# Kernel tuning notes

Hardware: AMD Instinct MI355X
Metric: run time of the kernel (lower is better)

The kernel has to match this reference:

```python
import jax, jax.numpy as jnp
import numpy as np

N_NODES = 50000
N_EDGES = 800000
IN_F = 128
HID = 128
N_REL = 8


def setup_inputs() -> dict:
    key = jax.random.key(0)
    ks = jax.random.split(key, 12)
    s = 0.05
    return {
        "in_feat": jax.random.normal(ks[0], (N_NODES, IN_F), dtype=jnp.float32),
        "W1": jax.random.normal(ks[1], (N_REL, IN_F, HID), dtype=jnp.float32) * s,
        "W1_self": jax.random.normal(ks[2], (IN_F, HID), dtype=jnp.float32) * s,
        "b1": jnp.zeros((HID,), dtype=jnp.float32),
        "W2": jax.random.normal(ks[3], (N_REL, HID, HID), dtype=jnp.float32) * s,
        "W2_self": jax.random.normal(ks[4], (HID, HID), dtype=jnp.float32) * s,
        "b2": jnp.zeros((HID,), dtype=jnp.float32),
        "fc_w": jax.random.normal(ks[5], (HID, 1), dtype=jnp.float32) * s,
        "fc_b": jnp.zeros((1,), dtype=jnp.float32),
        "src": jax.random.randint(ks[6], (N_EDGES,), 0, N_NODES),
        "dst": jax.random.randint(ks[7], (N_EDGES,), 0, N_NODES),
        "etypes": jax.random.randint(ks[8], (N_EDGES,), 0, N_REL),
    }


def _rel_graph_conv(h, W, W_self, b, src, dst, etypes, n_nodes):
    # Transform node features once per relation: [R, N, H]
    xr = jnp.einsum('nd,rdh->rnh', h, W)
    # Per-edge message: gather relation-specific transformed source features [E, H]
    msgs = xr[etypes, src]
    # Scatter-sum aggregation to destination nodes [N, H]
    agg = jax.ops.segment_sum(msgs, dst, num_segments=n_nodes)
    # Self-loop + bias + ReLU (DGL RelGraphConv defaults)
    return jax.nn.relu(agg + h @ W_self + b)


def reference(in_feat, W1, W1_self, b1, W2, W2_self, b2, fc_w, fc_b, src, dst, etypes):
    n = in_feat.shape[0]
    h = _rel_graph_conv(in_feat, W1, W1_self, b1, src, dst, etypes, n)
    # dropout layers are identity in eval mode
    h = _rel_graph_conv(h, W2, W2_self, b2, src, dst, etypes, n)
    pooled = jnp.mean(h, axis=0, keepdims=True)  # AvgPooling over one graph -> [1, H]
    logits = pooled @ fc_w + fc_b                # [1, 1]
    return jax.nn.sigmoid(logits)
```

## Files before the change

### kernel.cpp

```cpp
#include <hip/hip_runtime.h>

#define NNODES 50000
#define NEDGES 800000
#define F 128
#define NREL 8
#define NOUT 1152
#define NBKT 98
#define BSH 9
#define SEG 16384
#define NTILES 391
#define GEMM_BLOCKS (8 * 9 * 49)
#define CSR_BLOCKS 196

typedef float f32x4 __attribute__((ext_vector_type(4)));
typedef float f32x2 __attribute__((ext_vector_type(2)));

typedef __attribute__((address_space(3))) void lds_void;
typedef const __attribute__((address_space(1))) void glb_void;
__device__ __forceinline__ void gll16(const void* g, void* l) {
  __builtin_amdgcn_global_load_lds(
      (glb_void*)(unsigned long long)g,
      (lds_void*)(unsigned)(unsigned long long)l, 16, 0, 0);
}

#define PREP_ZERO  33
#define PREP_CVT   6250
#define PREP_W     144
__global__ __launch_bounds__(256)
void k_prep(const float* __restrict__ in_feat, unsigned* __restrict__ feat0,
            const float* __restrict__ W1, const float* __restrict__ W1s,
            unsigned* __restrict__ Wt1,
            const float* __restrict__ W2, const float* __restrict__ W2s,
            unsigned* __restrict__ Wt2,
            float* __restrict__ pooled_p, int* __restrict__ bcur) {
  const int b = blockIdx.x, t = threadIdx.x;
  if (b < 32) {
    pooled_p[b * 256 + t] = 0.f;
  } else if (b < PREP_ZERO) {
    if (t <= NBKT) bcur[t] = 0;
  } else if (b < PREP_ZERO + PREP_CVT) {
    int i = (b - PREP_ZERO) * 256 + t;
    float4 v = ((const float4*)in_feat)[i];
    unsigned pk = 0;
    pk = __builtin_amdgcn_cvt_pk_fp8_f32(v.x, v.y, pk, false);
    pk = __builtin_amdgcn_cvt_pk_fp8_f32(v.z, v.w, pk, true);
    feat0[i] = pk;
  } else {
    int w2 = (b >= PREP_ZERO + PREP_CVT + PREP_W);
    int idx = (b - PREP_ZERO - PREP_CVT - (w2 ? PREP_W : 0)) * 256 + t;
    int n = idx >> 5, k0 = (idx & 31) * 4;
    int r = n >> 7, c = n & 127;
    const float* Wr = w2 ? W2 : W1;
    const float* Ws = w2 ? W2s : W1s;
    float v0, v1, v2, v3;
    if (r < NREL) {
      v0 = Wr[((size_t)(r * F + k0 + 0)) * F + c];
      v1 = Wr[((size_t)(r * F + k0 + 1)) * F + c];
      v2 = Wr[((size_t)(r * F + k0 + 2)) * F + c];
      v3 = Wr[((size_t)(r * F + k0 + 3)) * F + c];
    } else {
      v0 = Ws[(size_t)(k0 + 0) * F + c];
      v1 = Ws[(size_t)(k0 + 1) * F + c];
      v2 = Ws[(size_t)(k0 + 2) * F + c];
      v3 = Ws[(size_t)(k0 + 3) * F + c];
    }
    unsigned pk = 0;
    pk = __builtin_amdgcn_cvt_pk_fp8_f32(v0, v1, pk, false);
    pk = __builtin_amdgcn_cvt_pk_fp8_f32(v2, v3, pk, true);
    (w2 ? Wt2 : Wt1)[idx] = pk;
  }
}

__global__ __launch_bounds__(512)
void k_fsort(const int* __restrict__ ebuf, const int* __restrict__ bcur,
             int* __restrict__ rowptr, int* __restrict__ edata) {
  __shared__ int cnt[512];
  __shared__ int pos[512];
  __shared__ int ws2[512];
  __shared__ int bc_s;
  const int b = blockIdx.x, t = threadIdx.x;
  int myc = (t < NBKT) ? bcur[t] : 0;
  ws2[t] = (t < b) ? myc : 0;
  if (t == b) bc_s = myc;
  __syncthreads();
  for (int off = 1; off < 512; off <<= 1) {
    int x = (t >= off) ? ws2[t - off] : 0;
    __syncthreads();
    ws2[t] += x;
    __syncthreads();
  }
  const int beg = ws2[511];
  const int cntb = bc_s;
  const int sbeg = b * SEG;

  cnt[t] = 0;
  __syncthreads();
  for (int e = t; e < cntb; e += 512)
    atomicAdd(&cnt[((unsigned)ebuf[sbeg + e]) >> 19], 1);
  __syncthreads();
  int myn = cnt[t];
  ws2[t] = myn;
  __syncthreads();
  for (int off = 1; off < 512; off <<= 1) {
    int x = (t >= off) ? ws2[t - off] : 0;
    __syncthreads();
    ws2[t] += x;
    __syncthreads();
  }
  pos[t] = ws2[t] - myn;
  __syncthreads();
  int node = (b << BSH) + t;
  if (node < NNODES) rowptr[node] = beg + pos[t];
  if (b == NBKT - 1 && t == 0) rowptr[NNODES] = NEDGES;
  __syncthreads();
  for (int e = t; e < cntb; e += 512) {
    int rec = ebuf[sbeg + e];
    int c = ((unsigned)rec) >> 19;
    int lrank = atomicAdd(&pos[c], 1);
    int srcv = (rec >> 3) & 0xFFFF;
    int etv = rec & 7;
    edata[beg + lrank] = srcv * NOUT + etv * F;
  }
}

__global__ __launch_bounds__(512, 8)
void gemm_xrs(const unsigned char* __restrict__ A,
              const unsigned char* __restrict__ Wt,
              unsigned char* __restrict__ xrs, int doCsr,
              const int* __restrict__ src, const int* __restrict__ dst,
              const int* __restrict__ et, int* __restrict__ bcur,
              int* __restrict__ ebuf) {
  __shared__ uint4 As[1024];
  __shared__ uint4 Bs[1024];
  __shared__ int lhist[NBKT];
  __shared__ int lbase[NBKT];
  const int tid = threadIdx.x;

  if (doCsr && blockIdx.x < CSR_BLOCKS) {
    if (tid < NBKT) lhist[tid] = 0;
    __syncthreads();
    int e0 = blockIdx.x * 4096;
    int rec[8], cc[8], lr[8];
#pragma unroll
    for (int i = 0; i < 8; ++i) {
      int e = e0 + tid + i * 512;
      if (e < NEDGES) {
        int d = dst[e];
        cc[i] = d >> BSH;
        rec[i] = ((d & 511) << 19) | (src[e] << 3) | et[e];
        lr[i] = atomicAdd(&lhist[cc[i]], 1);
      } else {
        cc[i] = -1;
      }
    }
    __syncthreads();
    if (tid < NBKT && lhist[tid] > 0) lbase[tid] = atomicAdd(&bcur[tid], lhist[tid]);
    __syncthreads();
#pragma unroll
    for (int i = 0; i < 8; ++i)
      if (cc[i] >= 0) ebuf[cc[i] * SEG + lbase[cc[i]] + lr[i]] = rec[i];
    return;
  }

  const int id = blockIdx.x - (doCsr ? CSR_BLOCKS : 0);
  const int x = id & 7, j = id >> 3;
  const int tile = (j / 9) * 8 + x;
  const int cb = j % 9;
  if (tile >= NTILES) return;
  const int row0 = tile * 128;

  const int lane = tid & 63;
  const int w = tid >> 6;
  const int i16 = lane & 15, q = lane >> 4;
  const int mbase = (w & 3) * 32, nbase = (w >> 2) * 64;

#pragma unroll
  for (int i = 0; i < 2; ++i) {
    int L = tid + i * 512;
    int r = L >> 3, c8s = L & 7;
    int c8 = c8s ^ (r & 7);
    int agr = row0 + r; if (agr >= NNODES) agr = NNODES - 1;
    gll16((const void*)(A + (size_t)agr * F + c8 * 16), (void*)&As[L]);
    gll16((const void*)(Wt + ((size_t)cb * 128 + r) * F + c8 * 16), (void*)&Bs[L]);
  }
  __syncthreads();

  f32x4 acc[2][4];
#pragma unroll
  for (int a = 0; a < 2; ++a)
#pragma unroll
    for (int b = 0; b < 4; ++b) acc[a][b] = (f32x4)0.f;

  const char* Ab = (const char*)As;
  const char* Bb = (const char*)Bs;
#pragma unroll
  for (int c = 0; c < 4; ++c) {
    const int ch = c * 2 + (q >> 1);
    const int h8 = (q & 1) << 3;
    long af[2], bfr[4];
#pragma unroll
    for (int mi = 0; mi < 2; ++mi) {
      int r = mbase + mi * 16 + i16;
      af[mi] = *(const long*)(Ab + r * 128 + ((ch ^ (r & 7)) << 4) + h8);
    }
#pragma unroll
    for (int ni = 0; ni < 4; ++ni) {
      int r = nbase + ni * 16 + i16;
      bfr[ni] = *(const long*)(Bb + r * 128 + ((ch ^ (r & 7)) << 4) + h8);
    }
#pragma unroll
    for (int mi = 0; mi < 2; ++mi)
#pragma unroll
      for (int ni = 0; ni < 4; ++ni)
        acc[mi][ni] = __builtin_amdgcn_mfma_f32_16x16x32_fp8_fp8(
            bfr[ni], af[mi], acc[mi][ni], 0, 0, 0);
  }

  unsigned pkv[2][4];
#pragma unroll
  for (int mi = 0; mi < 2; ++mi)
#pragma unroll
    for (int ni = 0; ni < 4; ++ni) {
      f32x4 v = acc[mi][ni];
      unsigned pk = 0;
      pk = __builtin_amdgcn_cvt_pk_fp8_f32(v[0], v[1], pk, false);
      pk = __builtin_amdgcn_cvt_pk_fp8_f32(v[2], v[3], pk, true);
      pkv[mi][ni] = pk;
    }

  __syncthreads();
  unsigned* sbuf = (unsigned*)As;
  {
    const int dbase = (nbase >> 2) + q;
#pragma unroll
    for (int mi = 0; mi < 2; ++mi) {
      int nl = mbase + mi * 16 + i16;
      int sw = (nl & 7) << 2;
      int vb_ = nl * 32;
#pragma unroll
      for (int ni = 0; ni < 4; ++ni)
        sbuf[vb_ + ((dbase + ni * 4) ^ sw)] = pkv[mi][ni];
    }
  }
  __syncthreads();

#pragma unroll
  for (int k = 0; k < 2; ++k) {
    int nl = k * 64 + (tid >> 3);
    int ch = tid & 7;
    int d0 = (ch * 4) ^ ((nl & 7) << 2);
    uint4 v = *(const uint4*)&sbuf[nl * 32 + d0];
    int row = row0 + nl;
    if (row < NNODES)
      *(uint4*)(xrs + (size_t)row * NOUT + cb * 128 + ch * 16) = v;
  }
}

__global__ __launch_bounds__(256)
void k_aggregate(const unsigned char* __restrict__ xrs,
                 const int* __restrict__ rowptr, const int* __restrict__ edata,
                 const float* __restrict__ bias, unsigned char* __restrict__ hout,
                 float* __restrict__ pooled_p) {
  __shared__ float red[8][128];
  const int wv = threadIdx.x >> 6;
  const int lane = threadIdx.x & 63;
  const int h = lane >> 5;
  const int sl = lane & 31;
  const int g = sl >> 3, s8 = sl & 7;
  const int node = blockIdx.x * 8 + wv * 2 + h;
  const int beg = rowptr[node], end = rowptr[node + 1];

  float a[16];
#pragma unroll
  for (int j = 0; j < 16; ++j) a[j] = 0.f;

#define ACC4(word, o_) { \
    f32x2 lo_ = __builtin_amdgcn_cvt_pk_f32_fp8((word), false); \
    f32x2 hi_ = __builtin_amdgcn_cvt_pk_f32_fp8((word), true);  \
    a[(o_) + 0] += lo_[0]; a[(o_) + 1] += lo_[1];               \
    a[(o_) + 2] += hi_[0]; a[(o_) + 3] += hi_[1]; }
#define ACC16(v_) { ACC4((v_).x, 0) ACC4((v_).y, 4) ACC4((v_).z, 8) ACC4((v_).w, 12) }

  if (g == 0) {
    uint4 sv = *(const uint4*)(xrs + (size_t)node * NOUT + NREL * F + s8 * 16);
    ACC16(sv)
  }

  for (int base = beg; base < end; base += 32) {
    int cnt = end - base; if (cnt > 32) cnt = 32;
    int my = (base + sl < end) ? edata[base + sl] : 0;
    int nfull = cnt >> 2, tail = cnt & 3;
    for (int qb = 0; qb < nfull; qb += 8) {
      int nq = nfull - qb; if (nq > 8) nq = 8;
      uint4 v[8];
#pragma unroll
      for (int k = 0; k < 8; ++k) {
        if (k < nq) {
          int off = __shfl(my, 4 * (qb + k) + g, 32);
          v[k] = *(const uint4*)(xrs + (size_t)off + s8 * 16);
        }
      }
#pragma unroll
      for (int k = 0; k < 8; ++k) {
        if (k < nq) ACC16(v[k])
      }
    }
    if (tail) {
      int e = 4 * nfull + g;
      int off = __shfl(my, (e < cnt) ? e : 0, 32);
      if (g < tail) {
        uint4 vv = *(const uint4*)(xrs + (size_t)off + s8 * 16);
        ACC16(vv)
      }
    }
  }

#pragma unroll
  for (int j = 0; j < 16; ++j) {
    a[j] += __shfl_xor(a[j], 8, 64);
    a[j] += __shfl_xor(a[j], 16, 64);
  }

#pragma unroll
  for (int i = 0; i < 4; ++i) {
    float4 bb = ((const float4*)bias)[s8 * 4 + i];
    a[i * 4 + 0] = fmaxf(a[i * 4 + 0] + bb.x, 0.f);
    a[i * 4 + 1] = fmaxf(a[i * 4 + 1] + bb.y, 0.f);
    a[i * 4 + 2] = fmaxf(a[i * 4 + 2] + bb.z, 0.f);
    a[i * 4 + 3] = fmaxf(a[i * 4 + 3] + bb.w, 0.f);
  }

  if (hout) {
    if (g == 0) {
      unsigned pk[4];
#pragma unroll
      for (int i = 0; i < 4; ++i) {
        unsigned p = 0;
        p = __builtin_amdgcn_cvt_pk_fp8_f32(a[i * 4 + 0], a[i * 4 + 1], p, false);
        p = __builtin_amdgcn_cvt_pk_fp8_f32(a[i * 4 + 2], a[i * 4 + 3], p, true);
        pk[i] = p;
      }
      *(uint4*)(hout + (size_t)node * F + s8 * 16) =
          make_uint4(pk[0], pk[1], pk[2], pk[3]);
    }
  } else {
    if (g == 0) {
#pragma unroll
      for (int j = 0; j < 16; ++j) red[wv * 2 + h][s8 * 16 + j] = a[j];
    }
    __syncthreads();
    if (threadIdx.x < 128) {
      float sm = 0.f;
#pragma unroll
      for (int r = 0; r < 8; ++r) sm += red[r][threadIdx.x];
      atomicAdd(&pooled_p[(blockIdx.x & 63) * 128 + threadIdx.x], sm);
    }
  }
#undef ACC16
#undef ACC4
}

__global__ __launch_bounds__(128)
void k_final(const float* __restrict__ pooled_p, const float* __restrict__ fcw,
             const float* __restrict__ fcb, float* __restrict__ out) {
  __shared__ float s[128];
  int t = threadIdx.x;
  float acc = 0.f;
#pragma unroll 8
  for (int k = 0; k < 64; ++k) acc += pooled_p[k * 128 + t];
  s[t] = acc * (1.0f / (float)NNODES) * fcw[t];
  __syncthreads();
  if (t == 0) {
    float v = 0.f;
    for (int i = 0; i < 128; ++i) v += s[i];
    v += fcb[0];
    out[0] = 1.f / (1.f + expf(-v));
  }
}

extern "C" void kernel_launch(void* const* d_in, const int* in_sizes, int n_in,
                              void* d_out, int out_size, void* d_ws, size_t ws_size,
                              hipStream_t stream) {
  const float* in_feat = (const float*)d_in[0];
  const float* W1      = (const float*)d_in[1];
  const float* W1s     = (const float*)d_in[2];
  const float* b1      = (const float*)d_in[3];
  const float* W2      = (const float*)d_in[4];
  const float* W2s     = (const float*)d_in[5];
  const float* b2      = (const float*)d_in[6];
  const float* fcw     = (const float*)d_in[7];
  const float* fcb     = (const float*)d_in[8];
  const int*   src     = (const int*)d_in[9];
  const int*   dst     = (const int*)d_in[10];
  const int*   et      = (const int*)d_in[11];
  float* out = (float*)d_out;

  unsigned char* xrs = (unsigned char*)d_ws;
  unsigned char* feat0 = xrs + (size_t)NNODES * NOUT;
  unsigned char* h1  = feat0 + (size_t)NNODES * F;
  unsigned char* Wt1 = h1 + (size_t)NNODES * F;
  unsigned char* Wt2 = Wt1 + (size_t)NOUT * F;
  float* pooled_p = (float*)(Wt2 + (size_t)NOUT * F);
  int*   bcur   = (int*)(pooled_p + 64 * 128);
  int*   rowptr = bcur + NBKT + 1;
  int*   ebuf   = rowptr + NNODES + 2;
  int*   edata  = ebuf + NBKT * SEG;

  k_prep<<<PREP_ZERO + PREP_CVT + 2 * PREP_W, 256, 0, stream>>>(
      in_feat, (unsigned*)feat0, W1, W1s, (unsigned*)Wt1,
      W2, W2s, (unsigned*)Wt2, pooled_p, bcur);

  const int aggBlocks = NNODES / 8;

  gemm_xrs<<<CSR_BLOCKS + GEMM_BLOCKS, 512, 0, stream>>>(
      feat0, Wt1, xrs, 1, src, dst, et, bcur, ebuf);
  k_fsort<<<NBKT, 512, 0, stream>>>(ebuf, bcur, rowptr, edata);
  k_aggregate<<<aggBlocks, 256, 0, stream>>>(xrs, rowptr, edata, b1, h1, nullptr);
  gemm_xrs<<<GEMM_BLOCKS, 512, 0, stream>>>(
      h1, Wt2, xrs, 0, src, dst, et, bcur, ebuf);
  k_aggregate<<<aggBlocks, 256, 0, stream>>>(xrs, rowptr, edata, b2, nullptr, pooled_p);

  k_final<<<1, 128, 0, stream>>>(pooled_p, fcw, fcb, out);
}
```

Baseline: 198.9 us.

## Move edge bucketing into prep and fuse CSR sort into first GEMM launch

Edge bucketing by destination moves from the first GEMM launch into the prep kernel. The per-bucket sort that builds rowptr and edata now runs as extra blocks inside the first GEMM launch, reusing its LDS, so the separate k_fsort launch is gone and sorting overlaps the layer-1 transform. Zeroing of pooled and bucket counters moves to a hipMemsetAsync, and the final dot product uses a wavefront shuffle reduction. The cost is an extra memset node, and the sort blocks now share occupancy with GEMM blocks.

```diff
diff --git a/kernel.cpp b/kernel.cpp
--- a/kernel.cpp
+++ b/kernel.cpp
@@ -23,7 +23,6 @@
       (lds_void*)(unsigned)(unsigned long long)l, 16, 0, 0);
 }
 
-#define PREP_ZERO  33
 #define PREP_CVT   6250
 #define PREP_W     144
 __global__ __launch_bounds__(256)
@@ -32,22 +31,46 @@
             unsigned* __restrict__ Wt1,
             const float* __restrict__ W2, const float* __restrict__ W2s,
             unsigned* __restrict__ Wt2,
-            float* __restrict__ pooled_p, int* __restrict__ bcur) {
+            const int* __restrict__ src, const int* __restrict__ dst,
+            const int* __restrict__ et,
+            int* __restrict__ bcur, int* __restrict__ ebuf) {
   const int b = blockIdx.x, t = threadIdx.x;
-  if (b < 32) {
-    pooled_p[b * 256 + t] = 0.f;
-  } else if (b < PREP_ZERO) {
-    if (t <= NBKT) bcur[t] = 0;
-  } else if (b < PREP_ZERO + PREP_CVT) {
-    int i = (b - PREP_ZERO) * 256 + t;
+  if (b < CSR_BLOCKS) {
+    __shared__ int lhist[NBKT];
+    __shared__ int lbase[NBKT];
+    if (t < NBKT) lhist[t] = 0;
+    __syncthreads();
+    int e0 = b * 4096;
+    int rec[16], cc[16], lr[16];
+#pragma unroll
+    for (int i = 0; i < 16; ++i) {
+      int e = e0 + t + i * 256;
+      if (e < NEDGES) {
+        int d = dst[e];
+        cc[i] = d >> BSH;
+        rec[i] = ((d & 511) << 19) | (src[e] << 3) | et[e];
+        lr[i] = atomicAdd(&lhist[cc[i]], 1);
+      } else {
+        cc[i] = -1;
+      }
+    }
+    __syncthreads();
+    if (t < NBKT && lhist[t] > 0) lbase[t] = atomicAdd(&bcur[t], lhist[t]);
+    __syncthreads();
+#pragma unroll
+    for (int i = 0; i < 16; ++i)
+      if (cc[i] >= 0) ebuf[cc[i] * SEG + lbase[cc[i]] + lr[i]] = rec[i];
+  } else if (b < CSR_BLOCKS + PREP_CVT) {
+    int i = (b - CSR_BLOCKS) * 256 + t;
     float4 v = ((const float4*)in_feat)[i];
     unsigned pk = 0;
     pk = __builtin_amdgcn_cvt_pk_fp8_f32(v.x, v.y, pk, false);
     pk = __builtin_amdgcn_cvt_pk_fp8_f32(v.z, v.w, pk, true);
     feat0[i] = pk;
   } else {
-    int w2 = (b >= PREP_ZERO + PREP_CVT + PREP_W);
-    int idx = (b - PREP_ZERO - PREP_CVT - (w2 ? PREP_W : 0)) * 256 + t;
+    int rem = b - CSR_BLOCKS - PREP_CVT;
+    int w2 = rem >= PREP_W;
+    int idx = (rem - (w2 ? PREP_W : 0)) * 256 + t;
     int n = idx >> 5, k0 = (idx & 31) * 4;
     int r = n >> 7, c = n & 127;
     const float* Wr = w2 ? W2 : W1;
@@ -71,98 +94,68 @@
   }
 }
 
-__global__ __launch_bounds__(512)
-void k_fsort(const int* __restrict__ ebuf, const int* __restrict__ bcur,
-             int* __restrict__ rowptr, int* __restrict__ edata) {
-  __shared__ int cnt[512];
-  __shared__ int pos[512];
-  __shared__ int ws2[512];
-  __shared__ int bc_s;
-  const int b = blockIdx.x, t = threadIdx.x;
-  int myc = (t < NBKT) ? bcur[t] : 0;
-  ws2[t] = (t < b) ? myc : 0;
-  if (t == b) bc_s = myc;
-  __syncthreads();
-  for (int off = 1; off < 512; off <<= 1) {
-    int x = (t >= off) ? ws2[t - off] : 0;
-    __syncthreads();
-    ws2[t] += x;
-    __syncthreads();
-  }
-  const int beg = ws2[511];
-  const int cntb = bc_s;
-  const int sbeg = b * SEG;
-
-  cnt[t] = 0;
-  __syncthreads();
-  for (int e = t; e < cntb; e += 512)
-    atomicAdd(&cnt[((unsigned)ebuf[sbeg + e]) >> 19], 1);
-  __syncthreads();
-  int myn = cnt[t];
-  ws2[t] = myn;
-  __syncthreads();
-  for (int off = 1; off < 512; off <<= 1) {
-    int x = (t >= off) ? ws2[t - off] : 0;
-    __syncthreads();
-    ws2[t] += x;
-    __syncthreads();
-  }
-  pos[t] = ws2[t] - myn;
-  __syncthreads();
-  int node = (b << BSH) + t;
-  if (node < NNODES) rowptr[node] = beg + pos[t];
-  if (b == NBKT - 1 && t == 0) rowptr[NNODES] = NEDGES;
-  __syncthreads();
-  for (int e = t; e < cntb; e += 512) {
-    int rec = ebuf[sbeg + e];
-    int c = ((unsigned)rec) >> 19;
-    int lrank = atomicAdd(&pos[c], 1);
-    int srcv = (rec >> 3) & 0xFFFF;
-    int etv = rec & 7;
-    edata[beg + lrank] = srcv * NOUT + etv * F;
-  }
-}
-
 __global__ __launch_bounds__(512, 8)
 void gemm_xrs(const unsigned char* __restrict__ A,
               const unsigned char* __restrict__ Wt,
-              unsigned char* __restrict__ xrs, int doCsr,
-              const int* __restrict__ src, const int* __restrict__ dst,
-              const int* __restrict__ et, int* __restrict__ bcur,
-              int* __restrict__ ebuf) {
+              unsigned char* __restrict__ xrs, int doAux,
+              const int* __restrict__ ebuf, const int* __restrict__ bcur,
+              int* __restrict__ rowptr, int* __restrict__ edata) {
   __shared__ uint4 As[1024];
   __shared__ uint4 Bs[1024];
-  __shared__ int lhist[NBKT];
-  __shared__ int lbase[NBKT];
   const int tid = threadIdx.x;
 
-  if (doCsr && blockIdx.x < CSR_BLOCKS) {
-    if (tid < NBKT) lhist[tid] = 0;
-    __syncthreads();
-    int e0 = blockIdx.x * 4096;
-    int rec[8], cc[8], lr[8];
-#pragma unroll
-    for (int i = 0; i < 8; ++i) {
-      int e = e0 + tid + i * 512;
-      if (e < NEDGES) {
-        int d = dst[e];
-        cc[i] = d >> BSH;
-        rec[i] = ((d & 511) << 19) | (src[e] << 3) | et[e];
-        lr[i] = atomicAdd(&lhist[cc[i]], 1);
-      } else {
-        cc[i] = -1;
-      }
-    }
-    __syncthreads();
-    if (tid < NBKT && lhist[tid] > 0) lbase[tid] = atomicAdd(&bcur[tid], lhist[tid]);
-    __syncthreads();
-#pragma unroll
-    for (int i = 0; i < 8; ++i)
-      if (cc[i] >= 0) ebuf[cc[i] * SEG + lbase[cc[i]] + lr[i]] = rec[i];
+  if (doAux && blockIdx.x < NBKT) {
+    int* cnt = (int*)As;
+    int* pos = cnt + 512;
+    int* ws2 = pos + 512;
+    int* bcs = ws2 + 512;
+    const int b = blockIdx.x, t = tid;
+    int myc = (t < NBKT) ? bcur[t] : 0;
+    ws2[t] = (t < b) ? myc : 0;
+    if (t == b) *bcs = myc;
+    __syncthreads();
+    for (int off = 1; off < 512; off <<= 1) {
+      int x = (t >= off) ? ws2[t - off] : 0;
+      __syncthreads();
+      ws2[t] += x;
+      __syncthreads();
+    }
+    const int beg = ws2[511];
+    const int cntb = *bcs;
+    const int sbeg = b * SEG;
+
+    cnt[t] = 0;
+    __syncthreads();
+    for (int e = t; e < cntb; e += 512)
+      atomicAdd(&cnt[((unsigned)ebuf[sbeg + e]) >> 19], 1);
+    __syncthreads();
+    int myn = cnt[t];
+    ws2[t] = myn;
+    __syncthreads();
+    for (int off = 1; off < 512; off <<= 1) {
+      int x = (t >= off) ? ws2[t - off] : 0;
+      __syncthreads();
+      ws2[t] += x;
+      __syncthreads();
+    }
+    pos[t] = ws2[t] - myn;
+    __syncthreads();
+    int node = (b << BSH) + t;
+    if (node < NNODES) rowptr[node] = beg + pos[t];
+    if (b == NBKT - 1 && t == 0) rowptr[NNODES] = NEDGES;
+    __syncthreads();
+    for (int e = t; e < cntb; e += 512) {
+      int rec = ebuf[sbeg + e];
+      int c = ((unsigned)rec) >> 19;
+      int lrank = atomicAdd(&pos[c], 1);
+      int srcv = (rec >> 3) & 0xFFFF;
+      int etv = rec & 7;
+      edata[beg + lrank] = srcv * NOUT + etv * F;
+    }
     return;
   }
 
-  const int id = blockIdx.x - (doCsr ? CSR_BLOCKS : 0);
+  const int id = blockIdx.x - (doAux ? NBKT : 0);
   const int x = id & 7, j = id >> 3;
   const int tile = (j / 9) * 8 + x;
   const int cb = j % 9;
@@ -370,11 +363,18 @@
   for (int k = 0; k < 64; ++k) acc += pooled_p[k * 128 + t];
   s[t] = acc * (1.0f / (float)NNODES) * fcw[t];
   __syncthreads();
-  if (t == 0) {
-    float v = 0.f;
-    for (int i = 0; i < 128; ++i) v += s[i];
-    v += fcb[0];
-    out[0] = 1.f / (1.f + expf(-v));
+  if (t < 64) {
+    float x = s[t] + s[t + 64];
+    x += __shfl_down(x, 32, 64);
+    x += __shfl_down(x, 16, 64);
+    x += __shfl_down(x, 8, 64);
+    x += __shfl_down(x, 4, 64);
+    x += __shfl_down(x, 2, 64);
+    x += __shfl_down(x, 1, 64);
+    if (t == 0) {
+      float v = x + fcb[0];
+      out[0] = 1.f / (1.f + expf(-v));
+    }
   }
 }
 
@@ -406,18 +406,19 @@
   int*   ebuf   = rowptr + NNODES + 2;
   int*   edata  = ebuf + NBKT * SEG;
 
-  k_prep<<<PREP_ZERO + PREP_CVT + 2 * PREP_W, 256, 0, stream>>>(
+  hipMemsetAsync(pooled_p, 0, (64 * 128 + NBKT + 1) * sizeof(float), stream);
+
+  k_prep<<<CSR_BLOCKS + PREP_CVT + 2 * PREP_W, 256, 0, stream>>>(
       in_feat, (unsigned*)feat0, W1, W1s, (unsigned*)Wt1,
-      W2, W2s, (unsigned*)Wt2, pooled_p, bcur);
+      W2, W2s, (unsigned*)Wt2, src, dst, et, bcur, ebuf);
 
   const int aggBlocks = NNODES / 8;
 
-  gemm_xrs<<<CSR_BLOCKS + GEMM_BLOCKS, 512, 0, stream>>>(
-      feat0, Wt1, xrs, 1, src, dst, et, bcur, ebuf);
-  k_fsort<<<NBKT, 512, 0, stream>>>(ebuf, bcur, rowptr, edata);
+  gemm_xrs<<<NBKT + GEMM_BLOCKS, 512, 0, stream>>>(
+      feat0, Wt1, xrs, 1, ebuf, bcur, rowptr, edata);
   k_aggregate<<<aggBlocks, 256, 0, stream>>>(xrs, rowptr, edata, b1, h1, nullptr);
   gemm_xrs<<<GEMM_BLOCKS, 512, 0, stream>>>(
-      h1, Wt2, xrs, 0, src, dst, et, bcur, ebuf);
+      h1, Wt2, xrs, 0, ebuf, bcur, rowptr, edata);
   k_aggregate<<<aggBlocks, 256, 0, stream>>>(xrs, rowptr, edata, b2, nullptr, pooled_p);
 
   k_final<<<1, 128, 0, stream>>>(pooled_p, fcw, fcb, out);
```

Result: no change. 197.4 us (-0.8%).
